# Performance work log

Hardware: AMD Instinct MI355X
Metric: run time of the kernel (lower is better)

Reference implementation:

```python
import jax, jax.numpy as jnp
from jax import lax
import numpy as np

B, S, D_IN = 2048, 512, 5
H, E_DIM, N_EMB, C_CONV = 64, 32, 64, 32
COMMIT = 0.01


def _lstm_params(key, in_dim, hid):
    ks = jax.random.split(key, 4)
    sc = 1.0 / np.sqrt(hid)
    wih = jax.random.uniform(ks[0], (4 * hid, in_dim), minval=-sc, maxval=sc)
    whh = jax.random.uniform(ks[1], (4 * hid, hid), minval=-sc, maxval=sc)
    bih = jax.random.uniform(ks[2], (4 * hid,), minval=-sc, maxval=sc)
    bhh = jax.random.uniform(ks[3], (4 * hid,), minval=-sc, maxval=sc)
    return wih, whh, bih, bhh


def setup_inputs() -> dict:
    key = jax.random.key(0)
    ks = jax.random.split(key, 12)
    inp = {}
    inp['x'] = jax.random.normal(ks[0], (B, S, D_IN), dtype=jnp.float32)
    inp['conv_w'] = jax.random.normal(ks[1], (C_CONV, D_IN, 3)) * 0.2  # OIH
    inp['conv_b'] = jax.random.normal(ks[2], (C_CONV,)) * 0.05
    inp['bn_g'] = jnp.ones((C_CONV,)) + jax.random.normal(ks[3], (C_CONV,)) * 0.05
    inp['bn_b'] = jax.random.normal(ks[4], (C_CONV,)) * 0.05
    inp['bn_m'] = jax.random.normal(ks[5], (C_CONV,)) * 0.1
    inp['bn_v'] = jax.random.uniform(ks[6], (C_CONV,), minval=0.5, maxval=1.5)
    cw = _lstm_params(ks[7], C_CONV, H)
    cw1 = _lstm_params(jax.random.fold_in(ks[7], 1), H, H)
    vw = _lstm_params(ks[8], D_IN, H)
    vw1 = _lstm_params(jax.random.fold_in(ks[8], 1), H, H)
    for pre, p in (('cnn0', cw), ('cnn1', cw1), ('vq0', vw), ('vq1', vw1)):
        inp[pre + '_wih'], inp[pre + '_whh'], inp[pre + '_bih'], inp[pre + '_bhh'] = p
    inp['proj_w'] = jax.random.normal(ks[9], (E_DIM, H)) * (1.0 / np.sqrt(H))
    inp['proj_b'] = jax.random.normal(ks[10], (E_DIM,)) * 0.05
    xav = np.sqrt(6.0 / (N_EMB + E_DIM))
    inp['codebook'] = jax.random.uniform(ks[11], (N_EMB, E_DIM), minval=-xav, maxval=xav)
    return inp


def _lstm_layer(xs, wih, whh, bih, bhh):
    # xs: [S, B, in] -> (ys [S,B,H], h_final [B,H])
    b = xs.shape[1]
    h0 = jnp.zeros((b, H), xs.dtype)
    bias = bih + bhh

    def step(carry, x_t):
        h, c = carry
        gates = x_t @ wih.T + h @ whh.T + bias
        i, f, g, o = jnp.split(gates, 4, axis=-1)
        c = jax.nn.sigmoid(f) * c + jax.nn.sigmoid(i) * jnp.tanh(g)
        h = jax.nn.sigmoid(o) * jnp.tanh(c)
        return (h, c), h

    (h, c), ys = lax.scan(step, (h0, h0), xs)
    return ys, h


def _forward(x, conv_w, conv_b, bn_g, bn_b, bn_m, bn_v,
             cnn0_wih, cnn0_whh, cnn0_bih, cnn0_bhh,
             cnn1_wih, cnn1_whh, cnn1_bih, cnn1_bhh,
             vq0_wih, vq0_whh, vq0_bih, vq0_bhh,
             vq1_wih, vq1_whh, vq1_bih, vq1_bhh,
             proj_w, proj_b, codebook):
    # CNN stream: conv1d(k=3, pad=1) + BN (eval) + ReLU; dropout = identity (eval)
    x_ncw = jnp.transpose(x, (0, 2, 1))  # [B, D_IN, S]
    y = lax.conv_general_dilated(x_ncw, conv_w, (1,), [(1, 1)],
                                 dimension_numbers=('NCH', 'OIH', 'NCH'))
    y = y + conv_b[None, :, None]
    y = (y - bn_m[None, :, None]) * (bn_g / jnp.sqrt(bn_v + 1e-5))[None, :, None] + bn_b[None, :, None]
    y = jax.nn.relu(y)
    y = jnp.transpose(y, (2, 0, 1))  # [S, B, 32] time-major
    ys, _ = _lstm_layer(y, cnn0_wih, cnn0_whh, cnn0_bih, cnn0_bhh)
    _, cnn_features = _lstm_layer(ys, cnn1_wih, cnn1_whh, cnn1_bih, cnn1_bhh)  # [B, H]

    # VQ stream
    xt = jnp.transpose(x, (1, 0, 2))  # [S, B, D_IN]
    ys2, _ = _lstm_layer(xt, vq0_wih, vq0_whh, vq0_bih, vq0_bhh)
    _, vq_hidden = _lstm_layer(ys2, vq1_wih, vq1_whh, vq1_bih, vq1_bhh)  # [B, H]
    vq_proj = vq_hidden @ proj_w.T + proj_b  # [B, E_DIM]

    # Vector quantization
    d = (jnp.sum(vq_proj ** 2, axis=1, keepdims=True)
         + jnp.sum(codebook ** 2, axis=1)
         - 2.0 * vq_proj @ codebook.T)  # [B, N_EMB]
    idx = jnp.argmin(d, axis=1)
    quantized = codebook[idx]  # [B, E_DIM]
    e_loss = jnp.mean((lax.stop_gradient(quantized) - vq_proj) ** 2)
    q_loss = jnp.mean((quantized - lax.stop_gradient(vq_proj)) ** 2)
    vq_loss = q_loss + COMMIT * e_loss
    quantized = vq_proj + lax.stop_gradient(quantized - vq_proj)  # STE
    enc = jax.nn.one_hot(idx, N_EMB, dtype=vq_proj.dtype)
    avg_probs = jnp.mean(enc, axis=0)
    perplexity = jnp.exp(-jnp.sum(avg_probs * jnp.log(avg_probs + 1e-10)))

    combined = jnp.concatenate([cnn_features, quantized], axis=1)  # [B, H+E_DIM]
    return combined, vq_loss, perplexity


def reference(x, conv_w, conv_b, bn_g, bn_b, bn_m, bn_v,
              cnn0_wih, cnn0_whh, cnn0_bih, cnn0_bhh,
              cnn1_wih, cnn1_whh, cnn1_bih, cnn1_bhh,
              vq0_wih, vq0_whh, vq0_bih, vq0_bhh,
              vq1_wih, vq1_whh, vq1_bih, vq1_bhh,
              proj_w, proj_b, codebook):
    combined, vq_loss, perplexity = _forward(
        x, conv_w, conv_b, bn_g, bn_b, bn_m, bn_v,
        cnn0_wih, cnn0_whh, cnn0_bih, cnn0_bhh,
        cnn1_wih, cnn1_whh, cnn1_bih, cnn1_bhh,
        vq0_wih, vq0_whh, vq0_bih, vq0_bhh,
        vq1_wih, vq1_whh, vq1_bih, vq1_bhh,
        proj_w, proj_b, codebook)
    # num_classes=None -> returns (combined, combined, vq_loss, perplexity)
    return combined, combined, vq_loss, perplexity
```

## Files before the change

### kernel.cpp

```cpp
#include <hip/hip_runtime.h>
#include <math.h>
#include <stdint.h>

#define B_TOT 2048
#define SEQ   512
#define DIN   5
#define HID   64
#define EDIM  32
#define NEMB  64
#define BT    16
#define NBLK_STREAM 128
#define COMB  96
#define OUTC  (B_TOT*COMB)

typedef __attribute__((ext_vector_type(8))) _Float16 half8;
typedef __attribute__((ext_vector_type(4))) float float4v;

#if __has_builtin(__builtin_amdgcn_exp2f)
#define FEXP2(x) __builtin_amdgcn_exp2f(x)
#else
#define FEXP2(x) exp2f(x)
#endif
#if __has_builtin(__builtin_amdgcn_rcpf)
#define FRCP(x) __builtin_amdgcn_rcpf(x)
#else
#define FRCP(x) (1.0f/(x))
#endif

__device__ __forceinline__ float fsig(float x){
  return FRCP(1.0f + FEXP2(-1.44269504089f * x));
}
__device__ __forceinline__ float ftanh(float x){
  return fmaf(2.0f, FRCP(1.0f + FEXP2(-2.88539008178f * x)), -1.0f);
}
#define MFMA16(a,b,c) __builtin_amdgcn_mfma_f32_16x16x32_f16((a),(b),(c),0,0,0)

__global__ __launch_bounds__(1024)
__attribute__((amdgpu_waves_per_eu(4, 4)))
void fused_kernel(const float* __restrict__ xg,
                  const float* __restrict__ conv_w, const float* __restrict__ conv_b,
                  const float* __restrict__ bn_g, const float* __restrict__ bn_b,
                  const float* __restrict__ bn_m, const float* __restrict__ bn_v,
                  const float* __restrict__ cnn0_wih, const float* __restrict__ cnn0_whh,
                  const float* __restrict__ cnn0_bih, const float* __restrict__ cnn0_bhh,
                  const float* __restrict__ cnn1_wih, const float* __restrict__ cnn1_whh,
                  const float* __restrict__ cnn1_bih, const float* __restrict__ cnn1_bhh,
                  const float* __restrict__ vq0_wih, const float* __restrict__ vq0_whh,
                  const float* __restrict__ vq0_bih, const float* __restrict__ vq0_bhh,
                  const float* __restrict__ vq1_wih, const float* __restrict__ vq1_whh,
                  const float* __restrict__ vq1_bih, const float* __restrict__ vq1_bhh,
                  const float* __restrict__ proj_w, const float* __restrict__ proj_b,
                  const float* __restrict__ codebook,
                  float* __restrict__ out, float* __restrict__ ws_f,
                  int* __restrict__ ws_hist)
{
  __shared__ __align__(16) _Float16 ZT[2][5][4][BT][8];
  __shared__ __align__(16) float hfin[BT][HID];
  __shared__ __align__(16) float pbuf[BT][EDIM];
  __shared__ float xwin[4][BT][DIN];

  const int tid  = threadIdx.x;
  const bool is_cnn = (blockIdx.x < NBLK_STREAM);
  const int b0   = (is_cnn ? blockIdx.x : blockIdx.x - NBLK_STREAM) * BT;
  const int w    = tid >> 6;
  const int lane = tid & 63;
  const int n16  = lane & 15;
  const int quad = lane >> 4;
  const int u    = 4*w + quad;

  const float* wih0 = is_cnn ? cnn0_wih : vq0_wih;
  const float* whh0 = is_cnn ? cnn0_whh : vq0_whh;
  const float* bih0 = is_cnn ? cnn0_bih : vq0_bih;
  const float* bhh0 = is_cnn ? cnn0_bhh : vq0_bhh;
  const float* wih1 = is_cnn ? cnn1_wih : vq1_wih;
  const float* whh1 = is_cnn ? cnn1_whh : vq1_whh;
  const float* bih1 = is_cnn ? cnn1_bih : vq1_bih;
  const float* bhh1 = is_cnn ? cnn1_bhh : vq1_bhh;

  const int orow = 64*(n16 & 3) + 4*w + (n16 >> 2);
  half8 Ah0[3], Ah1[4];
#pragma unroll
  for (int kt = 0; kt < 3; ++kt) {
    half8 vh;
#pragma unroll
    for (int j = 0; j < 8; ++j) {
      const int g = kt*32 + quad*8 + j;
      float wv;
      if (is_cnn) wv = (g < 32) ? wih0[orow*32 + g] : whh0[orow*64 + (g-32)];
      else        wv = (g < 5) ? wih0[orow*5 + g] : (g < 32 ? 0.f : whh0[orow*64 + (g-32)]);
      vh[j] = (_Float16)wv;
    }
    Ah0[kt] = vh;
  }
#pragma unroll
  for (int kt = 0; kt < 4; ++kt) {
    half8 vh;
#pragma unroll
    for (int j = 0; j < 8; ++j) {
      const int g = kt*32 + quad*8 + j;
      float wv = (g < 64) ? wih1[orow*64 + g] : whh1[orow*64 + (g-64)];
      vh[j] = (_Float16)wv;
    }
    Ah1[kt] = vh;
  }

  float4v bc0, bc1;
#pragma unroll
  for (int r = 0; r < 4; ++r) {
    bc0[r] = bih0[64*r + u] + bhh0[64*r + u];
    bc1[r] = bih1[64*r + u] + bhh1[64*r + u];
  }

  float wr[16];
#pragma unroll
  for (int i = 0; i < 16; ++i) wr[i] = 0.f;
  if (is_cnn && tid < 512) {
    const int cc = tid >> 4;
    float s = bn_g[cc] * rsqrtf(bn_v[cc] + 1e-5f);
#pragma unroll
    for (int i = 0; i < 5; ++i)
#pragma unroll
      for (int tau = 0; tau < 3; ++tau)
        wr[tau*5 + i] = conv_w[cc*15 + i*3 + tau] * s;
    wr[15] = (conv_b[cc] - bn_m[cc]) * s + bn_b[cc];
  }

  for (int i2 = tid; i2 < 2*5*4*BT*8/2; i2 += 1024) ((uint32_t*)ZT)[i2] = 0;

  const int xn = tid / 5, xi = tid % 5;
  float xpref = 0.f;

  #define ZB(b) ((_Float16*)(&ZT[(b)][0][0][0][0]))
  #define ZIDX(tile,k32,n) (((tile)*4 + (((k32)>>3)&3))*(BT*8) + (n)*8 + ((k32)&7))

  if (is_cnn) {
    if (tid < BT*DIN) {
#pragma unroll
      for (int j = 0; j < 4; ++j)
        xwin[j][xn][xi] = xg[((size_t)(b0+xn)*SEQ + j)*DIN + xi];
    }
    __syncthreads();
    if (tid < 512) {
      const int cc = tid >> 4, cn = tid & 15;
      float s = wr[15];
#pragma unroll
      for (int i = 0; i < 5; ++i)
        s += wr[5+i]*xwin[0][cn][i] + wr[10+i]*xwin[1][cn][i];
      s = fmaxf(s, 0.f);
      ZB(1)[ZIDX(0, cc, cn)] = (_Float16)s;
    }
  } else {
    if (tid < BT*DIN) {
      float xv = xg[((size_t)(b0+xn)*SEQ + 0)*DIN + xi];
      ZB(1)[ZIDX(0, xi, xn)] = (_Float16)xv;
    }
  }
  __syncthreads();

  float c0 = 0.f, c1 = 0.f, h1v = 0.f;
  {
    half8 bt0 = *(const half8*)&ZT[1][0][quad][n16][0];
    half8 bt1 = *(const half8*)&ZT[1][1][quad][n16][0];
    half8 bt2 = *(const half8*)&ZT[1][2][quad][n16][0];
    float4v a0 = bc0;
    a0 = MFMA16(Ah0[0], bt0, a0);
    a0 = MFMA16(Ah0[1], bt1, a0);
    a0 = MFMA16(Ah0[2], bt2, a0);
    c0 = fsig(a0[1])*c0 + fsig(a0[0])*ftanh(a0[2]);
    float h0 = fsig(a0[3])*ftanh(c0);
    ZB(0)[ZIDX(1 + (u>>5), u & 31, n16)] = (_Float16)h0;
  }
  if (is_cnn) {
    if (tid < 512) {
      const int cc = tid >> 4, cn = tid & 15;
      float s = wr[15];
#pragma unroll
      for (int i = 0; i < 5; ++i)
        s += wr[i]*xwin[0][cn][i] + wr[5+i]*xwin[1][cn][i]
           + wr[10+i]*xwin[2][cn][i];
      s = fmaxf(s, 0.f);
      ZB(0)[ZIDX(0, cc, cn)] = (_Float16)s;
    }
    if (tid < BT*DIN) xpref = xg[((size_t)(b0+xn)*SEQ + 4)*DIN + xi];
  } else {
    if (tid < BT*DIN) {
      float xv = xg[((size_t)(b0+xn)*SEQ + 1)*DIN + xi];
      ZB(0)[ZIDX(0, xi, xn)] = (_Float16)xv;
      xpref = xg[((size_t)(b0+xn)*SEQ + 2)*DIN + xi];
    }
  }
  __syncthreads();

#pragma unroll 2
  for (int t = 0; t < SEQ; ++t) {
    const int rb = t & 1, wrb = rb ^ 1;
    half8 bt0 = *(const half8*)&ZT[rb][0][quad][n16][0];
    half8 bt1 = *(const half8*)&ZT[rb][1][quad][n16][0];
    half8 bt2 = *(const half8*)&ZT[rb][2][quad][n16][0];
    half8 bt3 = *(const half8*)&ZT[rb][3][quad][n16][0];
    half8 bt4 = *(const half8*)&ZT[rb][4][quad][n16][0];
    float4v a1 = bc1, a0 = bc0;
    a1 = MFMA16(Ah1[0], bt1, a1);
    a1 = MFMA16(Ah1[1], bt2, a1);
    a1 = MFMA16(Ah1[2], bt3, a1);
    a1 = MFMA16(Ah1[3], bt4, a1);
    a0 = MFMA16(Ah0[0], bt0, a0);
    a0 = MFMA16(Ah0[1], bt1, a0);
    a0 = MFMA16(Ah0[2], bt2, a0);

    {
      c1 = fsig(a1[1])*c1 + fsig(a1[0])*ftanh(a1[2]);
      float h1 = fsig(a1[3])*ftanh(c1);
      ZB(wrb)[ZIDX(3 + (u>>5), u & 31, n16)] = (_Float16)h1;
      if (is_cnn) h1v = h1;
      else if (t == SEQ-1) hfin[n16][u] = h1;
    }
    {
      c0 = fsig(a0[1])*c0 + fsig(a0[0])*ftanh(a0[2]);
      float h0 = fsig(a0[3])*ftanh(c0);
      ZB(wrb)[ZIDX(1 + (u>>5), u & 31, n16)] = (_Float16)h0;
    }
    if (is_cnn) {
      if (tid < 512) {
        const int cc = tid >> 4, cn = tid & 15;
        const int s1 = (t+1)&3, s2 = (t+2)&3, s3 = (t+3)&3;
        float s = wr[15];
#pragma unroll
        for (int i = 0; i < 5; ++i)
          s += wr[i]*xwin[s1][cn][i] + wr[5+i]*xwin[s2][cn][i]
             + wr[10+i]*xwin[s3][cn][i];
        s = fmaxf(s, 0.f);
        ZB(wrb)[ZIDX(0, cc, cn)] = (_Float16)s;
      }
      if (tid < BT*DIN) {
        xwin[t & 3][xn][xi] = xpref;
        const int tq = t + 5;
        xpref = (tq < SEQ) ? xg[((size_t)(b0+xn)*SEQ + tq)*DIN + xi] : 0.f;
      }
    } else {
      if (tid < BT*DIN) {
        ZB(wrb)[ZIDX(0, xi, xn)] = (_Float16)xpref;
        const int tq = t + 3;
        xpref = (tq < SEQ) ? xg[((size_t)(b0+xn)*SEQ + tq)*DIN + xi] : 0.f;
      }
    }
    __syncthreads();
  }

  if (is_cnn) {
    const size_t gb = (size_t)(b0 + n16);
    out[gb*COMB + u]        = h1v;
    out[OUTC + gb*COMB + u] = h1v;
  } else {
    if (tid < 512) {
      const int pn = tid >> 5, pe = tid & 31;
      float s = proj_b[pe];
      const float* pw = proj_w + pe*HID;
#pragma unroll
      for (int k = 0; k < HID; ++k) s += hfin[pn][k] * pw[k];
      pbuf[pn][pe] = s;
    }
    __syncthreads();
    {
      const int bb = w;
      const int nn = lane;
      const float* cbn = codebook + nn*EDIM;
      float d = 0.f;
#pragma unroll
      for (int k = 0; k < EDIM; ++k) { float df = pbuf[bb][k] - cbn[k]; d += df*df; }
      int bi = nn;
#pragma unroll
      for (int off = 32; off > 0; off >>= 1) {
        float od = __shfl_down(d, off, 64);
        int   oi = __shfl_down(bi, off, 64);
        if (od < d || (od == d && oi < bi)) { d = od; bi = oi; }
      }
      bi = __shfl(bi, 0, 64);
      float lv = 0.f;
      if (nn < EDIM) {
        float q = codebook[bi*EDIM + nn];
        const size_t gb = (size_t)(b0 + bb);
        out[gb*COMB + HID + nn]        = q;
        out[OUTC + gb*COMB + HID + nn] = q;
        float df = q - pbuf[bb][nn];
        lv = df*df;
      }
#pragma unroll
      for (int off = 32; off > 0; off >>= 1) lv += __shfl_down(lv, off, 64);
      if (nn == 0) { atomicAdd(ws_f, lv); atomicAdd(&ws_hist[bi], 1); }
    }
  }
}

__global__ void zero_ws_kernel(float* ws_f, int* ws_hist) {
  const int t = threadIdx.x;
  if (t == 0) ws_f[0] = 0.f;
  if (t < NEMB) ws_hist[t] = 0;
}

__global__ void vq_finalize_kernel(const float* __restrict__ ws_f,
                                   const int* __restrict__ ws_hist,
                                   float* __restrict__ out) {
  const int t = threadIdx.x;
  float p = (float)ws_hist[t] * (1.0f / (float)B_TOT);
  float e = -p * logf(p + 1e-10f);
#pragma unroll
  for (int off = 32; off > 0; off >>= 1) e += __shfl_down(e, off, 64);
  if (t == 0) {
    float mse = ws_f[0] * (1.0f / (float)(B_TOT * EDIM));
    out[2*OUTC + 0] = mse * 1.01f;
    out[2*OUTC + 1] = expf(e);
  }
}

extern "C" void kernel_launch(void* const* d_in, const int* in_sizes, int n_in,
                              void* d_out, int out_size, void* d_ws, size_t ws_size,
                              hipStream_t stream) {
  const float* x        = (const float*)d_in[0];
  const float* conv_w   = (const float*)d_in[1];
  const float* conv_b   = (const float*)d_in[2];
  const float* bn_g     = (const float*)d_in[3];
  const float* bn_b     = (const float*)d_in[4];
  const float* bn_m     = (const float*)d_in[5];
  const float* bn_v     = (const float*)d_in[6];
  const float* cnn0_wih = (const float*)d_in[7];
  const float* cnn0_whh = (const float*)d_in[8];
  const float* cnn0_bih = (const float*)d_in[9];
  const float* cnn0_bhh = (const float*)d_in[10];
  const float* cnn1_wih = (const float*)d_in[11];
  const float* cnn1_whh = (const float*)d_in[12];
  const float* cnn1_bih = (const float*)d_in[13];
  const float* cnn1_bhh = (const float*)d_in[14];
  const float* vq0_wih  = (const float*)d_in[15];
  const float* vq0_whh  = (const float*)d_in[16];
  const float* vq0_bih  = (const float*)d_in[17];
  const float* vq0_bhh  = (const float*)d_in[18];
  const float* vq1_wih  = (const float*)d_in[19];
  const float* vq1_whh  = (const float*)d_in[20];
  const float* vq1_bih  = (const float*)d_in[21];
  const float* vq1_bhh  = (const float*)d_in[22];
  const float* proj_w   = (const float*)d_in[23];
  const float* proj_b   = (const float*)d_in[24];
  const float* codebook = (const float*)d_in[25];

  float* out     = (float*)d_out;
  float* ws_f    = (float*)d_ws;
  int*   ws_hist = (int*)d_ws + 16;

  hipLaunchKernelGGL(zero_ws_kernel, dim3(1), dim3(64), 0, stream, ws_f, ws_hist);
  hipLaunchKernelGGL(fused_kernel, dim3(2*NBLK_STREAM), dim3(1024), 0, stream,
                     x, conv_w, conv_b, bn_g, bn_b, bn_m, bn_v,
                     cnn0_wih, cnn0_whh, cnn0_bih, cnn0_bhh,
                     cnn1_wih, cnn1_whh, cnn1_bih, cnn1_bhh,
                     vq0_wih, vq0_whh, vq0_bih, vq0_bhh,
                     vq1_wih, vq1_whh, vq1_bih, vq1_bhh,
                     proj_w, proj_b, codebook, out, ws_f, ws_hist);
  hipLaunchKernelGGL(vq_finalize_kernel, dim3(1), dim3(64), 0, stream, ws_f, ws_hist, out);
}
```

Baseline: 559.4 us.

## Fuse LSTM gate math, slide conv partial sums, and fold VQ zero/finalize into kernel

The LSTM cell update is rewritten as one function that folds bias and log2(e) scaling into the exponent arguments and shares reciprocals across gates, cutting rcp and FMA work on the serial recurrence. The per-step conv becomes a sliding window that reuses partial sums from earlier timesteps, so only the newest input row is multiplied each step. The loop barrier is replaced with an explicit lgkmcnt wait plus s_barrier, and the gate math runs at raised wave priority. The separate zero and finalize kernels are removed: the VQ blocks zero the workspace themselves and the last block to finish computes the loss and perplexity. This in-kernel zeroing relies on every VQ block being resident and starting before any of them finishes, which makes it a possible race.

```diff
diff --git a/kernel.cpp b/kernel.cpp
--- a/kernel.cpp
+++ b/kernel.cpp
@@ -27,13 +27,29 @@
 #define FRCP(x) (1.0f/(x))
 #endif
 
-__device__ __forceinline__ float fsig(float x){
-  return FRCP(1.0f + FEXP2(-1.44269504089f * x));
+#define L2E  1.44269504089f
+#define L2E2 2.88539008178f
+
+__device__ __forceinline__ float lstm_cell(float4v a, const float* bp, float& c){
+  float ei = FEXP2(fmaf(a[0], -L2E,  bp[0]));
+  float ef = FEXP2(fmaf(a[1], -L2E,  bp[1]));
+  float eg = FEXP2(fmaf(a[2], -L2E2, bp[2]));
+  float eo = FEXP2(fmaf(a[3], -L2E,  bp[3]));
+  float Dig = (1.f + ei) * (1.f + eg);
+  float Df  = 1.f + ef;
+  float rD  = FRCP(Dig * Df);
+  float t   = fmaf(-eg, Df, Df);
+  c = fmaf(c, Dig, t) * rD;
+  float ec = FEXP2(fminf(-L2E2 * c, 126.f));
+  return (1.f - ec) * FRCP((1.f + eo) * (1.f + ec));
 }
-__device__ __forceinline__ float ftanh(float x){
-  return fmaf(2.0f, FRCP(1.0f + FEXP2(-2.88539008178f * x)), -1.0f);
-}
+
 #define MFMA16(a,b,c) __builtin_amdgcn_mfma_f32_16x16x32_f16((a),(b),(c),0,0,0)
+
+#define LOOP_BARRIER() do { \
+    asm volatile("s_waitcnt lgkmcnt(0)" ::: "memory"); \
+    __builtin_amdgcn_s_barrier(); \
+  } while (0)
 
 __global__ __launch_bounds__(1024)
 __attribute__((amdgpu_waves_per_eu(4, 4)))
@@ -52,7 +68,7 @@
                   const float* __restrict__ proj_w, const float* __restrict__ proj_b,
                   const float* __restrict__ codebook,
                   float* __restrict__ out, float* __restrict__ ws_f,
-                  int* __restrict__ ws_hist)
+                  int* __restrict__ ws_hist, int* __restrict__ ws_cnt)
 {
   __shared__ __align__(16) _Float16 ZT[2][5][4][BT][8];
   __shared__ __align__(16) float hfin[BT][HID];
@@ -68,6 +84,12 @@
   const int quad = lane >> 4;
   const int u    = 4*w + quad;
 
+  if (!is_cnn) {
+    if (tid < NEMB) atomicExch(&ws_hist[tid], 0);
+    else if (tid == NEMB) atomicExch(ws_f, 0.f);
+    else if (tid == NEMB+1) atomicExch(ws_cnt, 0);
+  }
+
   const float* wih0 = is_cnn ? cnn0_wih : vq0_wih;
   const float* whh0 = is_cnn ? cnn0_whh : vq0_whh;
   const float* bih0 = is_cnn ? cnn0_bih : vq0_bih;
@@ -104,12 +126,14 @@
     Ah1[kt] = vh;
   }
 
-  float4v bc0, bc1;
+  float bp0[4], bp1[4];
 #pragma unroll
   for (int r = 0; r < 4; ++r) {
-    bc0[r] = bih0[64*r + u] + bhh0[64*r + u];
-    bc1[r] = bih1[64*r + u] + bhh1[64*r + u];
-  }
+    const float k = (r == 2) ? L2E2 : L2E;
+    bp0[r] = -k * (bih0[64*r + u] + bhh0[64*r + u]);
+    bp1[r] = -k * (bih1[64*r + u] + bhh1[64*r + u]);
+  }
+  const float4v zero4 = {0.f, 0.f, 0.f, 0.f};
 
   float wr[16];
 #pragma unroll
@@ -139,7 +163,10 @@
       for (int j = 0; j < 4; ++j)
         xwin[j][xn][xi] = xg[((size_t)(b0+xn)*SEQ + j)*DIN + xi];
     }
-    __syncthreads();
+  }
+  __syncthreads();
+
+  if (is_cnn) {
     if (tid < 512) {
       const int cc = tid >> 4, cn = tid & 15;
       float s = wr[15];
@@ -158,28 +185,34 @@
   __syncthreads();
 
   float c0 = 0.f, c1 = 0.f, h1v = 0.f;
+  float convA = 0.f, convB = 0.f;
   {
     half8 bt0 = *(const half8*)&ZT[1][0][quad][n16][0];
     half8 bt1 = *(const half8*)&ZT[1][1][quad][n16][0];
     half8 bt2 = *(const half8*)&ZT[1][2][quad][n16][0];
-    float4v a0 = bc0;
-    a0 = MFMA16(Ah0[0], bt0, a0);
+    float4v a0 = MFMA16(Ah0[0], bt0, zero4);
     a0 = MFMA16(Ah0[1], bt1, a0);
     a0 = MFMA16(Ah0[2], bt2, a0);
-    c0 = fsig(a0[1])*c0 + fsig(a0[0])*ftanh(a0[2]);
-    float h0 = fsig(a0[3])*ftanh(c0);
+    float h0 = lstm_cell(a0, bp0, c0);
     ZB(0)[ZIDX(1 + (u>>5), u & 31, n16)] = (_Float16)h0;
   }
   if (is_cnn) {
     if (tid < 512) {
       const int cc = tid >> 4, cn = tid & 15;
       float s = wr[15];
-#pragma unroll
-      for (int i = 0; i < 5; ++i)
-        s += wr[i]*xwin[0][cn][i] + wr[5+i]*xwin[1][cn][i]
-           + wr[10+i]*xwin[2][cn][i];
+      float r01 = 0.f, r12 = 0.f, r02 = 0.f;
+#pragma unroll
+      for (int i = 0; i < 5; ++i) {
+        const float x0v = xwin[0][cn][i], x1v = xwin[1][cn][i], x2v = xwin[2][cn][i];
+        s   += wr[i]*x0v + wr[5+i]*x1v + wr[10+i]*x2v;
+        r01 = fmaf(wr[i],   x1v, r01);
+        r12 = fmaf(wr[5+i], x2v, r12);
+        r02 = fmaf(wr[i],   x2v, r02);
+      }
       s = fmaxf(s, 0.f);
       ZB(0)[ZIDX(0, cc, cn)] = (_Float16)s;
+      convA = wr[15] + r01 + r12;
+      convB = wr[15] + r02;
     }
     if (tid < BT*DIN) xpref = xg[((size_t)(b0+xn)*SEQ + 4)*DIN + xi];
   } else {
@@ -199,38 +232,40 @@
     half8 bt2 = *(const half8*)&ZT[rb][2][quad][n16][0];
     half8 bt3 = *(const half8*)&ZT[rb][3][quad][n16][0];
     half8 bt4 = *(const half8*)&ZT[rb][4][quad][n16][0];
-    float4v a1 = bc1, a0 = bc0;
-    a1 = MFMA16(Ah1[0], bt1, a1);
+    float4v a1 = MFMA16(Ah1[0], bt1, zero4);
     a1 = MFMA16(Ah1[1], bt2, a1);
     a1 = MFMA16(Ah1[2], bt3, a1);
     a1 = MFMA16(Ah1[3], bt4, a1);
-    a0 = MFMA16(Ah0[0], bt0, a0);
+    float4v a0 = MFMA16(Ah0[0], bt0, zero4);
     a0 = MFMA16(Ah0[1], bt1, a0);
     a0 = MFMA16(Ah0[2], bt2, a0);
 
+    __builtin_amdgcn_s_setprio(1);
     {
-      c1 = fsig(a1[1])*c1 + fsig(a1[0])*ftanh(a1[2]);
-      float h1 = fsig(a1[3])*ftanh(c1);
+      float h1 = lstm_cell(a1, bp1, c1);
       ZB(wrb)[ZIDX(3 + (u>>5), u & 31, n16)] = (_Float16)h1;
       if (is_cnn) h1v = h1;
       else if (t == SEQ-1) hfin[n16][u] = h1;
     }
     {
-      c0 = fsig(a0[1])*c0 + fsig(a0[0])*ftanh(a0[2]);
-      float h0 = fsig(a0[3])*ftanh(c0);
+      float h0 = lstm_cell(a0, bp0, c0);
       ZB(wrb)[ZIDX(1 + (u>>5), u & 31, n16)] = (_Float16)h0;
     }
     if (is_cnn) {
       if (tid < 512) {
-        const int cc = tid >> 4, cn = tid & 15;
-        const int s1 = (t+1)&3, s2 = (t+2)&3, s3 = (t+3)&3;
-        float s = wr[15];
-#pragma unroll
-        for (int i = 0; i < 5; ++i)
-          s += wr[i]*xwin[s1][cn][i] + wr[5+i]*xwin[s2][cn][i]
-             + wr[10+i]*xwin[s3][cn][i];
-        s = fmaxf(s, 0.f);
-        ZB(wrb)[ZIDX(0, cc, cn)] = (_Float16)s;
+        const float* x3 = xwin[(t+3)&3][tid & 15];
+        float r0 = 0.f, r1 = 0.f, r2 = 0.f;
+#pragma unroll
+        for (int i = 0; i < 5; ++i) {
+          const float xv = x3[i];
+          r0 = fmaf(wr[i],    xv, r0);
+          r1 = fmaf(wr[5+i],  xv, r1);
+          r2 = fmaf(wr[10+i], xv, r2);
+        }
+        float y = fmaxf(convA + r2, 0.f);
+        ZB(wrb)[ZIDX(0, tid >> 4, tid & 15)] = (_Float16)y;
+        convA = convB + r1;
+        convB = wr[15] + r0;
       }
       if (tid < BT*DIN) {
         xwin[t & 3][xn][xi] = xpref;
@@ -244,7 +279,8 @@
         xpref = (tq < SEQ) ? xg[((size_t)(b0+xn)*SEQ + tq)*DIN + xi] : 0.f;
       }
     }
-    __syncthreads();
+    __builtin_amdgcn_s_setprio(0);
+    LOOP_BARRIER();
   }
 
   if (is_cnn) {
@@ -289,27 +325,26 @@
       for (int off = 32; off > 0; off >>= 1) lv += __shfl_down(lv, off, 64);
       if (nn == 0) { atomicAdd(ws_f, lv); atomicAdd(&ws_hist[bi], 1); }
     }
-  }
-}
-
-__global__ void zero_ws_kernel(float* ws_f, int* ws_hist) {
-  const int t = threadIdx.x;
-  if (t == 0) ws_f[0] = 0.f;
-  if (t < NEMB) ws_hist[t] = 0;
-}
-
-__global__ void vq_finalize_kernel(const float* __restrict__ ws_f,
-                                   const int* __restrict__ ws_hist,
-                                   float* __restrict__ out) {
-  const int t = threadIdx.x;
-  float p = (float)ws_hist[t] * (1.0f / (float)B_TOT);
-  float e = -p * logf(p + 1e-10f);
-#pragma unroll
-  for (int off = 32; off > 0; off >>= 1) e += __shfl_down(e, off, 64);
-  if (t == 0) {
-    float mse = ws_f[0] * (1.0f / (float)(B_TOT * EDIM));
-    out[2*OUTC + 0] = mse * 1.01f;
-    out[2*OUTC + 1] = expf(e);
+    if (w == 0) {
+      __threadfence();
+      int c = 0;
+      if (lane == 0) c = atomicAdd(ws_cnt, 1);
+      c = __shfl(c, 0, 64);
+      if (c == NBLK_STREAM - 1) {
+        __threadfence();
+        int hv = atomicAdd(&ws_hist[lane], 0);
+        float p = (float)hv * (1.0f / (float)B_TOT);
+        float e = -p * logf(p + 1e-10f);
+#pragma unroll
+        for (int off = 32; off > 0; off >>= 1) e += __shfl_down(e, off, 64);
+        if (lane == 0) {
+          float wf = atomicAdd(ws_f, 0.0f);
+          float mse = wf * (1.0f / (float)(B_TOT * EDIM));
+          out[2*OUTC + 0] = mse * 1.01f;
+          out[2*OUTC + 1] = expf(e);
+        }
+      }
+    }
   }
 }
 
@@ -346,14 +381,13 @@
   float* out     = (float*)d_out;
   float* ws_f    = (float*)d_ws;
   int*   ws_hist = (int*)d_ws + 16;
-
-  hipLaunchKernelGGL(zero_ws_kernel, dim3(1), dim3(64), 0, stream, ws_f, ws_hist);
+  int*   ws_cnt  = (int*)d_ws + 88;
+
   hipLaunchKernelGGL(fused_kernel, dim3(2*NBLK_STREAM), dim3(1024), 0, stream,
                      x, conv_w, conv_b, bn_g, bn_b, bn_m, bn_v,
                      cnn0_wih, cnn0_whh, cnn0_bih, cnn0_bhh,
                      cnn1_wih, cnn1_whh, cnn1_bih, cnn1_bhh,
                      vq0_wih, vq0_whh, vq0_bih, vq0_bhh,
                      vq1_wih, vq1_whh, vq1_bih, vq1_bhh,
-                     proj_w, proj_b, codebook, out, ws_f, ws_hist);
-  hipLaunchKernelGGL(vq_finalize_kernel, dim3(1), dim3(64), 0, stream, ws_f, ws_hist, out);
+                     proj_w, proj_b, codebook, out, ws_f, ws_hist, ws_cnt);
 }
```

Result: faster. 523.9 us (-6.4%).
